# Kernel optimization log

Hardware: AMD Instinct MI355X
Metric: run time of the kernel (lower is better)

Reference implementation:

```python
import jax, jax.numpy as jnp
import numpy as np

B, S, N, M = 64, 512, 512, 128   # batch, sensory_size, state_size, motor_size
UNFOLDS = 6
DT = 0.1  # elapsed_time


def _gate(v, mu, sigma):
    # piecewise-linear 'sigmoid': clip((v - mu + sigma) / (2 sigma), 0, 1)
    # v: [B, P] -> [B, P, 1] broadcast against [P, N]
    return jnp.clip((v[..., None] - mu + sigma) / (2.0 * sigma), 0.0, 1.0)


def setup_inputs() -> dict:
    key = jax.random.key(0)
    ks = jax.random.split(key, 12)
    u = lambda k, sh, lo, hi: jax.random.uniform(k, sh, jnp.float32, lo, hi)
    inputs = jax.random.normal(ks[0], (B, S), dtype=jnp.float32)
    states = jax.random.normal(ks[1], (B, N), dtype=jnp.float32) * 0.1
    # parameters per _init_ranges
    tau = u(ks[2], (N,), 0.001, 2.0)
    b = u(ks[3], (N,), -0.2, 0.2)
    erev = jnp.where(jax.random.bernoulli(ks[4], 0.8, (N, N)), 1.0, -1.0).astype(jnp.float32)
    w = u(ks[5], (N, N), 0.001, 1.0)
    sigma = jnp.full((N, N), 0.5, jnp.float32)
    mu = jnp.full((N, N), 0.5, jnp.float32)
    sensory_erev = jnp.where(jax.random.bernoulli(ks[6], 0.8, (S, N)), 1.0, -1.0).astype(jnp.float32)
    sensory_w = u(ks[7], (S, N), 0.001, 1.0)
    sensory_sigma = jnp.full((S, N), 0.5, jnp.float32)
    sensory_mu = jnp.full((S, N), 0.5, jnp.float32)
    sparsity_mask = jax.random.bernoulli(ks[8], 0.3, (N, N)).astype(jnp.float32)
    sensory_sparsity_mask = jax.random.bernoulli(ks[9], 0.3, (S, N)).astype(jnp.float32)
    input_w = jnp.ones((S,), jnp.float32)
    input_b = jnp.zeros((S,), jnp.float32)
    output_w = jnp.ones((M,), jnp.float32)
    output_b = jnp.zeros((M,), jnp.float32)
    return dict(inputs=inputs, states=states, tau=tau, b=b, erev=erev, w=w,
                sigma=sigma, mu=mu, sensory_erev=sensory_erev, sensory_w=sensory_w,
                sensory_sigma=sensory_sigma, sensory_mu=sensory_mu,
                sparsity_mask=sparsity_mask, sensory_sparsity_mask=sensory_sparsity_mask,
                input_w=input_w, input_b=input_b, output_w=output_w, output_b=output_b)


def reference(inputs, states, tau, b, erev, w, sigma, mu,
              sensory_erev, sensory_w, sensory_sigma, sensory_mu,
              sparsity_mask, sensory_sparsity_mask,
              input_w, input_b, output_w, output_b):
    # input mapping (affine)
    x = inputs * input_w + input_b                                   # [B, S]
    # sensory synapses, computed once
    sa = _gate(x, sensory_mu, sensory_sigma) * sensory_sparsity_mask  # [B, S, N]
    s_rev = jnp.einsum('bsn,sn->bn', sa, sensory_erev)               # [B, N]
    s_w = jnp.einsum('bsn,sn->bn', sa, sensory_w)                    # [B, N]
    delta = DT / UNFOLDS

    def step(v, _):
        g = _gate(v, mu, sigma) * sparsity_mask                      # [B, N, N]
        sum_rev = jnp.einsum('bij,ij->bj', g, erev) + s_rev + b      # sum over presynaptic i
        sum_w = jnp.einsum('bij,ij->bj', g, w) + s_w
        k = 1.0 / (1.0 + sum_w)
        taun = tau * k
        q = taun / (taun + delta)
        v_new = q * v + (1.0 - q) * k * sum_rev
        return v_new, None

    v, _ = jax.lax.scan(step, states, None, length=UNFOLDS)
    # output mapping: slice last M neurons (M < N), then affine
    out = v[:, -M:] * output_w + output_b                            # [B, M]
    return out, v
```

## Files before the change

### kernel.cpp

```cpp
#include <hip/hip_runtime.h>
#include <string.h>

constexpr int cB = 64, cS = 512, cN = 512, cM = 128, cUNF = 6;
constexpr float cDELTA = 0.016666666666666666f;

constexpr int KB = 4;
constexpr int JT = 32;
constexpr int NJT = cN / JT;
constexpr int NT = 1024;
constexpr int NW = NT / 64;
constexpr int NB = (cB / KB) * NJT;
constexpr int ILEN = 16;
constexpr int SLEN = 16;

constexpr size_t OFF_EWT = 0;
constexpr size_t OFF_SRB = (size_t)cN * cN * 2;
constexpr size_t OFF_SW  = OFF_SRB + (size_t)cB * cN;
constexpr size_t OFF_VA  = OFF_SW  + (size_t)cB * cN;
constexpr size_t OFF_VB  = OFF_VA  + (size_t)cB * cN;
constexpr size_t OFF_CTR = OFF_VB  + (size_t)cB * cN;
constexpr int SLOT_STRIDE = 16;

__device__ __forceinline__ float clamp01(float x) {
    return __builtin_amdgcn_fmed3f(x, 0.0f, 1.0f);
}

__global__ __launch_bounds__(NT)
void k_prep(const float* __restrict__ inputs, const float* __restrict__ bias,
            const float* __restrict__ erev,  const float* __restrict__ wgt,
            const float* __restrict__ sigma, const float* __restrict__ mu,
            const float* __restrict__ serev, const float* __restrict__ swgt,
            const float* __restrict__ ssigma,const float* __restrict__ smu,
            const float* __restrict__ mask,  const float* __restrict__ smask,
            const float* __restrict__ inw,   const float* __restrict__ inb,
            float* __restrict__ ws)
{
    float2* EWt  = (float2*)(ws + OFF_EWT);
    float*  srb  = ws + OFF_SRB;
    float*  swS  = ws + OFF_SW;
    int*    ctr  = (int*)(ws + OFF_CTR);
    int*    flags = ctr + 4096;

    const int tid = threadIdx.x, bid = blockIdx.x;
    const int bg = bid >> 4, jt = bid & (NJT - 1);
    const int b0 = bg * KB, j0 = jt * JT;
    const int jl = tid & (JT - 1), ic = tid >> 5;
    const int wv_id = tid >> 6, lane = tid & 63;
    const int j = j0 + jl;

    __shared__ float xsh[cS * KB];
    __shared__ float redR[KB * NW * JT];
    __shared__ float redW[KB * NW * JT];

    {
        int idx = bid * NT + tid;
        int i = idx >> 9, jj = idx & (cN - 1);
        int jtt = jj >> 5, jjl = jj & (JT - 1);
        float mk = mask[idx];
        float2 ew = make_float2(erev[idx] * mk, wgt[idx] * mk);
        unsigned long long bits;
        memcpy(&bits, &ew, 8);
        __hip_atomic_store(
            (unsigned long long*)&EWt[(size_t)jtt * (cN * JT) + i * JT + jjl],
            bits, __ATOMIC_RELAXED, __HIP_MEMORY_SCOPE_AGENT);
        if (mk != 0.0f && !((sigma[idx] == 0.5f) && (mu[idx] == 0.5f)))
            __hip_atomic_store(&flags[jtt], 1, __ATOMIC_RELAXED, __HIP_MEMORY_SCOPE_AGENT);
    }

#pragma unroll
    for (int r = 0; r < (cS * KB) / NT; ++r) {
        int t = tid + r * NT;
        int bb = t & 3, s = t >> 2;
        xsh[t] = fmaf(inputs[(b0 + bb) * cS + s], inw[s], inb[s]);
    }
    __syncthreads();

    {
        float aR[KB] = {0.f, 0.f, 0.f, 0.f}, aW[KB] = {0.f, 0.f, 0.f, 0.f};
        int idx = (ic * SLEN) * cN + j;
        int xo  = (ic * SLEN) * KB;
#pragma unroll 4
        for (int ii = 0; ii < SLEN; ++ii, idx += cN, xo += KB) {
            float sg = ssigma[idx];
            float a  = 0.5f / sg;
            float c  = fmaf(-smu[idx], a, 0.5f);
            float mk = smask[idx];
            float e  = serev[idx] * mk;
            float wv = swgt[idx] * mk;
            const float4 xv = *(const float4*)&xsh[xo];
            float g;
            g = clamp01(fmaf(xv.x, a, c)); aR[0] = fmaf(g, e, aR[0]); aW[0] = fmaf(g, wv, aW[0]);
            g = clamp01(fmaf(xv.y, a, c)); aR[1] = fmaf(g, e, aR[1]); aW[1] = fmaf(g, wv, aW[1]);
            g = clamp01(fmaf(xv.z, a, c)); aR[2] = fmaf(g, e, aR[2]); aW[2] = fmaf(g, wv, aW[2]);
            g = clamp01(fmaf(xv.w, a, c)); aR[3] = fmaf(g, e, aR[3]); aW[3] = fmaf(g, wv, aW[3]);
        }
#pragma unroll
        for (int b = 0; b < KB; ++b) {
            aR[b] += __shfl_xor(aR[b], 32, 64);
            aW[b] += __shfl_xor(aW[b], 32, 64);
        }
        if (lane < JT) {
#pragma unroll
            for (int b = 0; b < KB; ++b) {
                redR[(b * NW + wv_id) * JT + lane] = aR[b];
                redW[(b * NW + wv_id) * JT + lane] = aW[b];
            }
        }
    }
    __syncthreads();

    if (tid < JT * KB) {
        int jj = tid & (JT - 1), bb = tid >> 5;
        float r = 0.f, wv = 0.f;
#pragma unroll
        for (int w = 0; w < NW; ++w) {
            r  += redR[(bb * NW + w) * JT + jj];
            wv += redW[(bb * NW + w) * JT + jj];
        }
        int jg = j0 + jj;
        int gidx = (b0 + bb) * cN + jg;
        srb[gidx] = r + bias[jg];
        swS[gidx] = wv;
    }
}

__global__ __launch_bounds__(NT, 4)
void k_main(const float* __restrict__ states, const float* __restrict__ tau,
            const float* __restrict__ sigma,  const float* __restrict__ mu,
            const float* __restrict__ outw,   const float* __restrict__ outb,
            float* __restrict__ out, float* __restrict__ ws)
{
    const float* srb = ws + OFF_SRB;
    const float* swS = ws + OFF_SW;
    float* vA  = ws + OFF_VA;
    float* vB  = ws + OFF_VB;
    int*   ctr = (int*)(ws + OFF_CTR);

    const int tid = threadIdx.x, bid = blockIdx.x;
    const int jt = (bid & 7) * 2 + ((bid >> 3) & 1);
    const int bg = bid >> 4;
    const int b0 = bg * KB, j0 = jt * JT;
    const int jl = tid & (JT - 1), ic = tid >> 5;
    const int wv_id = tid >> 6, lane = tid & 63;
    int* mySlot  = ctr + (bg * 16 + jt) * SLOT_STRIDE;
    int* bgSlots = ctr + (bg * 16) * SLOT_STRIDE;
    const int* flags = ctr + 4096;

    const float2* ews = (const float2*)(ws + OFF_EWT) + (size_t)jt * (cN * JT);

    __shared__ float stage[cN * KB];
    __shared__ float redR[KB * NW * JT];
    __shared__ float redW[KB * NW * JT];

    const int fast = (flags[jt] != 1);

    float my_srb = 0.f, my_sw = 0.f, my_tau = 0.f, my_ow = 0.f, my_ob = 0.f;
    float vold = 0.f;
    int my_gidx = 0, my_mi = -1;
    if (tid < JT * KB) {
        int jj = tid & (JT - 1), bb = tid >> 5;
        int jg = j0 + jj;
        my_gidx = (b0 + bb) * cN + jg;
        my_srb  = srb[my_gidx];
        my_sw   = swS[my_gidx];
        my_tau  = tau[jg];
        vold    = states[my_gidx];
        if (jg >= cN - cM) {
            int m = jg - (cN - cM);
            my_ow = outw[m]; my_ob = outb[m];
            my_mi = (b0 + bb) * cM + m;
        }
    }

    const float* vin = states;
    for (int u = 0; u < cUNF; ++u) {
#pragma unroll
        for (int r = 0; r < (cN * KB) / NT; ++r) {
            int t = tid + r * NT;
            int bb = t >> 9, ii = t & (cN - 1);
            float vvv = __hip_atomic_load(&vin[(b0 + bb) * cN + ii],
                                          __ATOMIC_RELAXED, __HIP_MEMORY_SCOPE_AGENT);
            stage[ii * KB + bb] = fast ? clamp01(vvv) : vvv;
        }
        __syncthreads();

        float aR[KB] = {0.f, 0.f, 0.f, 0.f}, aW[KB] = {0.f, 0.f, 0.f, 0.f};
        if (fast) {
            int eo = (ic * ILEN) * JT + jl;
            int vo = (ic * ILEN) * KB;
#pragma unroll 8
            for (int ii = 0; ii < ILEN; ++ii, eo += JT, vo += KB) {
                const float2 ew = ews[eo];
                const float4 g4 = *(const float4*)&stage[vo];
                aR[0] = fmaf(g4.x, ew.x, aR[0]); aW[0] = fmaf(g4.x, ew.y, aW[0]);
                aR[1] = fmaf(g4.y, ew.x, aR[1]); aW[1] = fmaf(g4.y, ew.y, aW[1]);
                aR[2] = fmaf(g4.z, ew.x, aR[2]); aW[2] = fmaf(g4.z, ew.y, aW[2]);
                aR[3] = fmaf(g4.w, ew.x, aR[3]); aW[3] = fmaf(g4.w, ew.y, aW[3]);
            }
        } else {
            int j    = j0 + jl;
            int idx  = (ic * ILEN) * cN + j;
            int eo   = (ic * ILEN) * JT + jl;
            int vo   = (ic * ILEN) * KB;
#pragma unroll 4
            for (int ii = 0; ii < ILEN; ++ii, idx += cN, eo += JT, vo += KB) {
                float sg = sigma[idx];
                float a  = 0.5f / sg;
                float c  = fmaf(-mu[idx], a, 0.5f);
                const float2 ew = ews[eo];
                const float4 v4 = *(const float4*)&stage[vo];
                float g;
                g = clamp01(fmaf(v4.x, a, c)); aR[0] = fmaf(g, ew.x, aR[0]); aW[0] = fmaf(g, ew.y, aW[0]);
                g = clamp01(fmaf(v4.y, a, c)); aR[1] = fmaf(g, ew.x, aR[1]); aW[1] = fmaf(g, ew.y, aW[1]);
                g = clamp01(fmaf(v4.z, a, c)); aR[2] = fmaf(g, ew.x, aR[2]); aW[2] = fmaf(g, ew.y, aW[2]);
                g = clamp01(fmaf(v4.w, a, c)); aR[3] = fmaf(g, ew.x, aR[3]); aW[3] = fmaf(g, ew.y, aW[3]);
            }
        }
#pragma unroll
        for (int b = 0; b < KB; ++b) {
            aR[b] += __shfl_xor(aR[b], 32, 64);
            aW[b] += __shfl_xor(aW[b], 32, 64);
        }
        if (lane < JT) {
#pragma unroll
            for (int b = 0; b < KB; ++b) {
                redR[(b * NW + wv_id) * JT + lane] = aR[b];
                redW[(b * NW + wv_id) * JT + lane] = aW[b];
            }
        }
        __syncthreads();

        float* vout = (u & 1) ? vB : vA;
        if (tid < JT * KB) {
            int jj = tid & (JT - 1), bb = tid >> 5;
            float r = 0.f, wv = 0.f;
#pragma unroll
            for (int w = 0; w < NW; ++w) {
                r  += redR[(bb * NW + w) * JT + jj];
                wv += redW[(bb * NW + w) * JT + jj];
            }
            r  += my_srb;
            wv += my_sw;
            float k    = 1.0f / (1.0f + wv);
            float taun = my_tau * k;
            float inv  = 1.0f / (taun + cDELTA);
            float vn   = (taun * inv) * vold + (cDELTA * inv) * k * r;
            vold = vn;
            if (u == cUNF - 1) {
                (out + cB * cM)[my_gidx] = vn;
                if (my_mi >= 0) out[my_mi] = fmaf(vn, my_ow, my_ob);
            } else {
                __hip_atomic_store(&vout[my_gidx], vn,
                                   __ATOMIC_RELAXED, __HIP_MEMORY_SCOPE_AGENT);
            }
        }

        if (u < cUNF - 1) {
            __syncthreads();
            if (tid == 0)
                __hip_atomic_store(mySlot, u + 1,
                                   __ATOMIC_RELAXED, __HIP_MEMORY_SCOPE_AGENT);
            if (tid < NJT) {
                const int* slot = bgSlots + tid * SLOT_STRIDE;
                while (__hip_atomic_load(slot, __ATOMIC_RELAXED, __HIP_MEMORY_SCOPE_AGENT) < u + 1)
                    __builtin_amdgcn_s_sleep(1);
            }
            __syncthreads();
            vin = (u & 1) ? vB : vA;
        }
    }
}

extern "C" void kernel_launch(void* const* d_in, const int* in_sizes, int n_in,
                              void* d_out, int out_size, void* d_ws, size_t ws_size,
                              hipStream_t stream)
{
    const float* inputs = (const float*)d_in[0];
    const float* states = (const float*)d_in[1];
    const float* tau    = (const float*)d_in[2];
    const float* bias   = (const float*)d_in[3];
    const float* erev   = (const float*)d_in[4];
    const float* wgt    = (const float*)d_in[5];
    const float* sigma  = (const float*)d_in[6];
    const float* mu     = (const float*)d_in[7];
    const float* serev  = (const float*)d_in[8];
    const float* swgt   = (const float*)d_in[9];
    const float* ssigma = (const float*)d_in[10];
    const float* smu    = (const float*)d_in[11];
    const float* mask   = (const float*)d_in[12];
    const float* smask  = (const float*)d_in[13];
    const float* inw    = (const float*)d_in[14];
    const float* inb    = (const float*)d_in[15];
    const float* outw   = (const float*)d_in[16];
    const float* outb   = (const float*)d_in[17];
    float* out = (float*)d_out;
    float* ws  = (float*)d_ws;

    k_prep<<<NB, NT, 0, stream>>>(inputs, bias, erev, wgt, sigma, mu,
                                  serev, swgt, ssigma, smu, mask, smask,
                                  inw, inb, ws);

    k_main<<<NB, NT, 0, stream>>>(states, tau, sigma, mu,
                                  outw, outb, out, ws);
}
```

Baseline: 124.1 us.

## Fuse prep and main into one MFMA fp16 kernel with register-resident weights

```diff
diff --git a/kernel.cpp b/kernel.cpp
--- a/kernel.cpp
+++ b/kernel.cpp
@@ -4,270 +4,248 @@
 constexpr int cB = 64, cS = 512, cN = 512, cM = 128, cUNF = 6;
 constexpr float cDELTA = 0.016666666666666666f;
 
-constexpr int KB = 4;
-constexpr int JT = 32;
-constexpr int NJT = cN / JT;
-constexpr int NT = 1024;
-constexpr int NW = NT / 64;
-constexpr int NB = (cB / KB) * NJT;
-constexpr int ILEN = 16;
-constexpr int SLEN = 16;
-
-constexpr size_t OFF_EWT = 0;
-constexpr size_t OFF_SRB = (size_t)cN * cN * 2;
-constexpr size_t OFF_SW  = OFF_SRB + (size_t)cB * cN;
-constexpr size_t OFF_VA  = OFF_SW  + (size_t)cB * cN;
-constexpr size_t OFF_VB  = OFF_VA  + (size_t)cB * cN;
-constexpr size_t OFF_CTR = OFF_VB  + (size_t)cB * cN;
+constexpr int JT   = 16;
+constexpr int NBLK = cN / JT;
+constexpr int NT   = 256;
 constexpr int SLOT_STRIDE = 16;
+
+constexpr size_t OFF_V0   = 0;
+constexpr size_t OFF_V1   = (size_t)cB * cN;
+constexpr size_t OFF_SLOT = OFF_V1 + (size_t)cB * cN;
+
+typedef _Float16 half8 __attribute__((ext_vector_type(8)));
+typedef float    floatx4 __attribute__((ext_vector_type(4)));
 
 __device__ __forceinline__ float clamp01(float x) {
     return __builtin_amdgcn_fmed3f(x, 0.0f, 1.0f);
 }
 
-__global__ __launch_bounds__(NT)
-void k_prep(const float* __restrict__ inputs, const float* __restrict__ bias,
-            const float* __restrict__ erev,  const float* __restrict__ wgt,
-            const float* __restrict__ sigma, const float* __restrict__ mu,
-            const float* __restrict__ serev, const float* __restrict__ swgt,
-            const float* __restrict__ ssigma,const float* __restrict__ smu,
-            const float* __restrict__ mask,  const float* __restrict__ smask,
-            const float* __restrict__ inw,   const float* __restrict__ inb,
-            float* __restrict__ ws)
+__global__ __launch_bounds__(NT, 1)
+void k_fused(const float* __restrict__ inputs, const float* __restrict__ states,
+             const float* __restrict__ tau,    const float* __restrict__ bias,
+             const float* __restrict__ erev,   const float* __restrict__ wgt,
+             const float* __restrict__ sigma,  const float* __restrict__ mu,
+             const float* __restrict__ serev,  const float* __restrict__ swgt,
+             const float* __restrict__ ssigma, const float* __restrict__ smu,
+             const float* __restrict__ mask,   const float* __restrict__ smask,
+             const float* __restrict__ inw,    const float* __restrict__ inb,
+             const float* __restrict__ outw,   const float* __restrict__ outb,
+             float* __restrict__ out, float* __restrict__ ws)
 {
-    float2* EWt  = (float2*)(ws + OFF_EWT);
-    float*  srb  = ws + OFF_SRB;
-    float*  swS  = ws + OFF_SW;
-    int*    ctr  = (int*)(ws + OFF_CTR);
-    int*    flags = ctr + 4096;
-
-    const int tid = threadIdx.x, bid = blockIdx.x;
-    const int bg = bid >> 4, jt = bid & (NJT - 1);
-    const int b0 = bg * KB, j0 = jt * JT;
-    const int jl = tid & (JT - 1), ic = tid >> 5;
-    const int wv_id = tid >> 6, lane = tid & 63;
-    const int j = j0 + jl;
-
-    __shared__ float xsh[cS * KB];
-    __shared__ float redR[KB * NW * JT];
-    __shared__ float redW[KB * NW * JT];
+    float* v0 = ws + OFF_V0;
+    float* v1 = ws + OFF_V1;
+    int* slots = (int*)(ws + OFF_SLOT);
+
+    const int tid  = threadIdx.x;
+    const int blk  = blockIdx.x;
+    const int j0   = blk * JT;
+    const int lane = tid & 63;
+    const int mt   = tid >> 6;
+    const int lr   = lane & 15;
+    const int lg   = lane >> 4;
+    const int bj   = j0 + lr;
+    const int arow = mt * 16 + lr;
+    const int kbase = lg * 8;
+    const int cb0  = mt * 16 + lg * 4;
+
+    int* mySlot = slots + blk * SLOT_STRIDE;
+    __shared__ int flagR, flagS;
+
+    float vold[4];
+    const float tau_j  = tau[bj];
+    const float bias_j = bias[bj];
+    float ow = 0.f, ob = 0.f;
+    if (bj >= cN - cM) { ow = outw[bj - (cN - cM)]; ob = outb[bj - (cN - cM)]; }
+
+#pragma unroll
+    for (int r = 0; r < 4; ++r) {
+        vold[r] = states[(size_t)(cb0 + r) * cN + bj];
+        __hip_atomic_store(&v0[(size_t)(cb0 + r) * cN + bj], vold[r],
+                           __ATOMIC_RELAXED, __HIP_MEMORY_SCOPE_AGENT);
+    }
+    if (tid == 0) { flagR = 0; flagS = 0; }
+    __syncthreads();
+    if (tid == 0)
+        __hip_atomic_store(mySlot, 1, __ATOMIC_RELAXED, __HIP_MEMORY_SCOPE_AGENT);
 
     {
-        int idx = bid * NT + tid;
-        int i = idx >> 9, jj = idx & (cN - 1);
-        int jtt = jj >> 5, jjl = jj & (JT - 1);
-        float mk = mask[idx];
-        float2 ew = make_float2(erev[idx] * mk, wgt[idx] * mk);
-        unsigned long long bits;
-        memcpy(&bits, &ew, 8);
-        __hip_atomic_store(
-            (unsigned long long*)&EWt[(size_t)jtt * (cN * JT) + i * JT + jjl],
-            bits, __ATOMIC_RELAXED, __HIP_MEMORY_SCOPE_AGENT);
-        if (mk != 0.0f && !((sigma[idx] == 0.5f) && (mu[idx] == 0.5f)))
-            __hip_atomic_store(&flags[jtt], 1, __ATOMIC_RELAXED, __HIP_MEMORY_SCOPE_AGENT);
-    }
-
-#pragma unroll
-    for (int r = 0; r < (cS * KB) / NT; ++r) {
-        int t = tid + r * NT;
-        int bb = t & 3, s = t >> 2;
-        xsh[t] = fmaf(inputs[(b0 + bb) * cS + s], inw[s], inb[s]);
+        bool badR = false, badS = false;
+        const int jj = j0 + (tid & 15);
+        const int i0 = (tid >> 4) * 32;
+        for (int r = 0; r < 32; ++r) {
+            size_t o = (size_t)(i0 + r) * cN + jj;
+            if (mask[o]  != 0.f && (sigma[o]  != 0.5f || mu[o]  != 0.5f)) badR = true;
+            if (smask[o] != 0.f && (ssigma[o] != 0.5f || smu[o] != 0.5f)) badS = true;
+        }
+        if (badR) flagR = 1;
+        if (badS) flagS = 1;
     }
     __syncthreads();
-
-    {
-        float aR[KB] = {0.f, 0.f, 0.f, 0.f}, aW[KB] = {0.f, 0.f, 0.f, 0.f};
-        int idx = (ic * SLEN) * cN + j;
-        int xo  = (ic * SLEN) * KB;
-#pragma unroll 4
-        for (int ii = 0; ii < SLEN; ++ii, idx += cN, xo += KB) {
-            float sg = ssigma[idx];
+    const bool fastR = (flagR == 0), fastS = (flagS == 0);
+
+    float srb[4], swv[4];
+    half8 bE[16], bW[16];
+    if (fastS) {
+#pragma unroll
+        for (int kk = 0; kk < 16; ++kk) {
+            half8 e8, w8;
+#pragma unroll
+            for (int t = 0; t < 8; ++t) {
+                size_t o = (size_t)(kk * 32 + kbase + t) * cN + bj;
+                float mk = smask[o];
+                e8[t] = (_Float16)(serev[o] * mk);
+                w8[t] = (_Float16)(swgt[o] * mk);
+            }
+            bE[kk] = e8; bW[kk] = w8;
+        }
+        floatx4 aR = {0.f, 0.f, 0.f, 0.f}, aW = {0.f, 0.f, 0.f, 0.f};
+#pragma unroll
+        for (int kk = 0; kk < 16; ++kk) {
+            const float* xp = inputs + (size_t)arow * cS + kk * 32 + kbase;
+            const float* wp = inw + kk * 32 + kbase;
+            const float* bp = inb + kk * 32 + kbase;
+            half8 ax;
+#pragma unroll
+            for (int t = 0; t < 8; ++t)
+                ax[t] = (_Float16)clamp01(fmaf(xp[t], wp[t], bp[t]));
+            aR = __builtin_amdgcn_mfma_f32_16x16x32_f16(ax, bE[kk], aR, 0, 0, 0);
+            aW = __builtin_amdgcn_mfma_f32_16x16x32_f16(ax, bW[kk], aW, 0, 0, 0);
+        }
+#pragma unroll
+        for (int r = 0; r < 4; ++r) { srb[r] = aR[r] + bias_j; swv[r] = aW[r]; }
+    } else {
+        float sr4[4] = {0,0,0,0}, sw4[4] = {0,0,0,0};
+        for (int s = 0; s < cS; ++s) {
+            size_t o = (size_t)s * cN + bj;
+            float mk = smask[o];
+            float sg = ssigma[o];
             float a  = 0.5f / sg;
-            float c  = fmaf(-smu[idx], a, 0.5f);
-            float mk = smask[idx];
-            float e  = serev[idx] * mk;
-            float wv = swgt[idx] * mk;
-            const float4 xv = *(const float4*)&xsh[xo];
-            float g;
-            g = clamp01(fmaf(xv.x, a, c)); aR[0] = fmaf(g, e, aR[0]); aW[0] = fmaf(g, wv, aW[0]);
-            g = clamp01(fmaf(xv.y, a, c)); aR[1] = fmaf(g, e, aR[1]); aW[1] = fmaf(g, wv, aW[1]);
-            g = clamp01(fmaf(xv.z, a, c)); aR[2] = fmaf(g, e, aR[2]); aW[2] = fmaf(g, wv, aW[2]);
-            g = clamp01(fmaf(xv.w, a, c)); aR[3] = fmaf(g, e, aR[3]); aW[3] = fmaf(g, wv, aW[3]);
-        }
-#pragma unroll
-        for (int b = 0; b < KB; ++b) {
-            aR[b] += __shfl_xor(aR[b], 32, 64);
-            aW[b] += __shfl_xor(aW[b], 32, 64);
-        }
-        if (lane < JT) {
-#pragma unroll
-            for (int b = 0; b < KB; ++b) {
-                redR[(b * NW + wv_id) * JT + lane] = aR[b];
-                redW[(b * NW + wv_id) * JT + lane] = aW[b];
-            }
-        }
+            float c  = fmaf(-smu[o], a, 0.5f);
+            float ee = serev[o] * mk, ww = swgt[o] * mk;
+            float iw = inw[s], ib = inb[s];
+#pragma unroll
+            for (int r = 0; r < 4; ++r) {
+                float x = fmaf(inputs[(size_t)(cb0 + r) * cS + s], iw, ib);
+                float g = clamp01(fmaf(x, a, c));
+                sr4[r] = fmaf(g, ee, sr4[r]);
+                sw4[r] = fmaf(g, ww, sw4[r]);
+            }
+        }
+#pragma unroll
+        for (int r = 0; r < 4; ++r) { srb[r] = sr4[r] + bias_j; swv[r] = sw4[r]; }
+    }
+
+    if (fastR) {
+#pragma unroll
+        for (int kk = 0; kk < 16; ++kk) {
+            half8 e8, w8;
+#pragma unroll
+            for (int t = 0; t < 8; ++t) {
+                size_t o = (size_t)(kk * 32 + kbase + t) * cN + bj;
+                float mk = mask[o];
+                e8[t] = (_Float16)(erev[o] * mk);
+                w8[t] = (_Float16)(wgt[o] * mk);
+            }
+            bE[kk] = e8; bW[kk] = w8;
+        }
+    }
+
+    if (tid < NBLK) {
+        const int* sl = slots + tid * SLOT_STRIDE;
+        while (__hip_atomic_load(sl, __ATOMIC_RELAXED, __HIP_MEMORY_SCOPE_AGENT) < 1)
+            __builtin_amdgcn_s_sleep(1);
     }
     __syncthreads();
 
-    if (tid < JT * KB) {
-        int jj = tid & (JT - 1), bb = tid >> 5;
-        float r = 0.f, wv = 0.f;
-#pragma unroll
-        for (int w = 0; w < NW; ++w) {
-            r  += redR[(bb * NW + w) * JT + jj];
-            wv += redW[(bb * NW + w) * JT + jj];
-        }
-        int jg = j0 + jj;
-        int gidx = (b0 + bb) * cN + jg;
-        srb[gidx] = r + bias[jg];
-        swS[gidx] = wv;
-    }
-}
-
-__global__ __launch_bounds__(NT, 4)
-void k_main(const float* __restrict__ states, const float* __restrict__ tau,
-            const float* __restrict__ sigma,  const float* __restrict__ mu,
-            const float* __restrict__ outw,   const float* __restrict__ outb,
-            float* __restrict__ out, float* __restrict__ ws)
-{
-    const float* srb = ws + OFF_SRB;
-    const float* swS = ws + OFF_SW;
-    float* vA  = ws + OFF_VA;
-    float* vB  = ws + OFF_VB;
-    int*   ctr = (int*)(ws + OFF_CTR);
-
-    const int tid = threadIdx.x, bid = blockIdx.x;
-    const int jt = (bid & 7) * 2 + ((bid >> 3) & 1);
-    const int bg = bid >> 4;
-    const int b0 = bg * KB, j0 = jt * JT;
-    const int jl = tid & (JT - 1), ic = tid >> 5;
-    const int wv_id = tid >> 6, lane = tid & 63;
-    int* mySlot  = ctr + (bg * 16 + jt) * SLOT_STRIDE;
-    int* bgSlots = ctr + (bg * 16) * SLOT_STRIDE;
-    const int* flags = ctr + 4096;
-
-    const float2* ews = (const float2*)(ws + OFF_EWT) + (size_t)jt * (cN * JT);
-
-    __shared__ float stage[cN * KB];
-    __shared__ float redR[KB * NW * JT];
-    __shared__ float redW[KB * NW * JT];
-
-    const int fast = (flags[jt] != 1);
-
-    float my_srb = 0.f, my_sw = 0.f, my_tau = 0.f, my_ow = 0.f, my_ob = 0.f;
-    float vold = 0.f;
-    int my_gidx = 0, my_mi = -1;
-    if (tid < JT * KB) {
-        int jj = tid & (JT - 1), bb = tid >> 5;
-        int jg = j0 + jj;
-        my_gidx = (b0 + bb) * cN + jg;
-        my_srb  = srb[my_gidx];
-        my_sw   = swS[my_gidx];
-        my_tau  = tau[jg];
-        vold    = states[my_gidx];
-        if (jg >= cN - cM) {
-            int m = jg - (cN - cM);
-            my_ow = outw[m]; my_ob = outb[m];
-            my_mi = (b0 + bb) * cM + m;
-        }
-    }
-
-    const float* vin = states;
     for (int u = 0; u < cUNF; ++u) {
-#pragma unroll
-        for (int r = 0; r < (cN * KB) / NT; ++r) {
-            int t = tid + r * NT;
-            int bb = t >> 9, ii = t & (cN - 1);
-            float vvv = __hip_atomic_load(&vin[(b0 + bb) * cN + ii],
-                                          __ATOMIC_RELAXED, __HIP_MEMORY_SCOPE_AGENT);
-            stage[ii * KB + bb] = fast ? clamp01(vvv) : vvv;
-        }
-        __syncthreads();
-
-        float aR[KB] = {0.f, 0.f, 0.f, 0.f}, aW[KB] = {0.f, 0.f, 0.f, 0.f};
-        if (fast) {
-            int eo = (ic * ILEN) * JT + jl;
-            int vo = (ic * ILEN) * KB;
-#pragma unroll 8
-            for (int ii = 0; ii < ILEN; ++ii, eo += JT, vo += KB) {
-                const float2 ew = ews[eo];
-                const float4 g4 = *(const float4*)&stage[vo];
-                aR[0] = fmaf(g4.x, ew.x, aR[0]); aW[0] = fmaf(g4.x, ew.y, aW[0]);
-                aR[1] = fmaf(g4.y, ew.x, aR[1]); aW[1] = fmaf(g4.y, ew.y, aW[1]);
-                aR[2] = fmaf(g4.z, ew.x, aR[2]); aW[2] = fmaf(g4.z, ew.y, aW[2]);
-                aR[3] = fmaf(g4.w, ew.x, aR[3]); aW[3] = fmaf(g4.w, ew.y, aW[3]);
-            }
+        const float* vR = (u & 1) ? v1 : v0;
+        float*       vW = (u & 1) ? v0 : v1;
+
+        float sumE[4], sumW[4];
+        if (fastR) {
+            half8 ax[16];
+#pragma unroll
+            for (int kk = 0; kk < 16; ++kk) {
+                union { unsigned long long u[4]; float f[8]; } cv;
+                const unsigned long long* p = (const unsigned long long*)
+                    (vR + (size_t)arow * cN + kk * 32 + kbase);
+                cv.u[0] = __hip_atomic_load(p + 0, __ATOMIC_RELAXED, __HIP_MEMORY_SCOPE_AGENT);
+                cv.u[1] = __hip_atomic_load(p + 1, __ATOMIC_RELAXED, __HIP_MEMORY_SCOPE_AGENT);
+                cv.u[2] = __hip_atomic_load(p + 2, __ATOMIC_RELAXED, __HIP_MEMORY_SCOPE_AGENT);
+                cv.u[3] = __hip_atomic_load(p + 3, __ATOMIC_RELAXED, __HIP_MEMORY_SCOPE_AGENT);
+                half8 a8;
+#pragma unroll
+                for (int t = 0; t < 8; ++t)
+                    a8[t] = (_Float16)clamp01(cv.f[t]);
+                ax[kk] = a8;
+            }
+            floatx4 aE = {0.f, 0.f, 0.f, 0.f}, aWc = {0.f, 0.f, 0.f, 0.f};
+#pragma unroll
+            for (int kk = 0; kk < 16; ++kk) {
+                aE  = __builtin_amdgcn_mfma_f32_16x16x32_f16(ax[kk], bE[kk], aE,  0, 0, 0);
+                aWc = __builtin_amdgcn_mfma_f32_16x16x32_f16(ax[kk], bW[kk], aWc, 0, 0, 0);
+            }
+#pragma unroll
+            for (int r = 0; r < 4; ++r) { sumE[r] = aE[r]; sumW[r] = aWc[r]; }
         } else {
-            int j    = j0 + jl;
-            int idx  = (ic * ILEN) * cN + j;
-            int eo   = (ic * ILEN) * JT + jl;
-            int vo   = (ic * ILEN) * KB;
-#pragma unroll 4
-            for (int ii = 0; ii < ILEN; ++ii, idx += cN, eo += JT, vo += KB) {
-                float sg = sigma[idx];
+            float r4[4] = {0,0,0,0}, w4[4] = {0,0,0,0};
+            for (int i = 0; i < cN; ++i) {
+                size_t o = (size_t)i * cN + bj;
+                float mk = mask[o];
+                float sg = sigma[o];
                 float a  = 0.5f / sg;
-                float c  = fmaf(-mu[idx], a, 0.5f);
-                const float2 ew = ews[eo];
-                const float4 v4 = *(const float4*)&stage[vo];
-                float g;
-                g = clamp01(fmaf(v4.x, a, c)); aR[0] = fmaf(g, ew.x, aR[0]); aW[0] = fmaf(g, ew.y, aW[0]);
-                g = clamp01(fmaf(v4.y, a, c)); aR[1] = fmaf(g, ew.x, aR[1]); aW[1] = fmaf(g, ew.y, aW[1]);
-                g = clamp01(fmaf(v4.z, a, c)); aR[2] = fmaf(g, ew.x, aR[2]); aW[2] = fmaf(g, ew.y, aW[2]);
-                g = clamp01(fmaf(v4.w, a, c)); aR[3] = fmaf(g, ew.x, aR[3]); aW[3] = fmaf(g, ew.y, aW[3]);
-            }
-        }
-#pragma unroll
-        for (int b = 0; b < KB; ++b) {
-            aR[b] += __shfl_xor(aR[b], 32, 64);
-            aW[b] += __shfl_xor(aW[b], 32, 64);
-        }
-        if (lane < JT) {
-#pragma unroll
-            for (int b = 0; b < KB; ++b) {
-                redR[(b * NW + wv_id) * JT + lane] = aR[b];
-                redW[(b * NW + wv_id) * JT + lane] = aW[b];
-            }
-        }
-        __syncthreads();
-
-        float* vout = (u & 1) ? vB : vA;
-        if (tid < JT * KB) {
-            int jj = tid & (JT - 1), bb = tid >> 5;
-            float r = 0.f, wv = 0.f;
-#pragma unroll
-            for (int w = 0; w < NW; ++w) {
-                r  += redR[(bb * NW + w) * JT + jj];
-                wv += redW[(bb * NW + w) * JT + jj];
-            }
-            r  += my_srb;
-            wv += my_sw;
-            float k    = 1.0f / (1.0f + wv);
-            float taun = my_tau * k;
+                float c  = fmaf(-mu[o], a, 0.5f);
+                float ee = erev[o] * mk, ww = wgt[o] * mk;
+#pragma unroll
+                for (int r = 0; r < 4; ++r) {
+                    float vi = __hip_atomic_load(&vR[(size_t)(cb0 + r) * cN + i],
+                                                 __ATOMIC_RELAXED, __HIP_MEMORY_SCOPE_AGENT);
+                    float g = clamp01(fmaf(vi, a, c));
+                    r4[r] = fmaf(g, ee, r4[r]);
+                    w4[r] = fmaf(g, ww, w4[r]);
+                }
+            }
+#pragma unroll
+            for (int r = 0; r < 4; ++r) { sumE[r] = r4[r]; sumW[r] = w4[r]; }
+        }
+
+#pragma unroll
+        for (int r = 0; r < 4; ++r) {
+            float rr   = sumE[r] + srb[r];
+            float wsum = sumW[r] + swv[r];
+            float k    = 1.0f / (1.0f + wsum);
+            float taun = tau_j * k;
             float inv  = 1.0f / (taun + cDELTA);
-            float vn   = (taun * inv) * vold + (cDELTA * inv) * k * r;
-            vold = vn;
-            if (u == cUNF - 1) {
-                (out + cB * cM)[my_gidx] = vn;
-                if (my_mi >= 0) out[my_mi] = fmaf(vn, my_ow, my_ob);
-            } else {
-                __hip_atomic_store(&vout[my_gidx], vn,
+            float vn   = (taun * inv) * vold[r] + (cDELTA * inv) * k * rr;
+            vold[r] = vn;
+        }
+
+        if (u < cUNF - 1) {
+#pragma unroll
+            for (int r = 0; r < 4; ++r)
+                __hip_atomic_store(&vW[(size_t)(cb0 + r) * cN + bj], vold[r],
                                    __ATOMIC_RELAXED, __HIP_MEMORY_SCOPE_AGENT);
-            }
-        }
-
-        if (u < cUNF - 1) {
             __syncthreads();
             if (tid == 0)
-                __hip_atomic_store(mySlot, u + 1,
+                __hip_atomic_store(mySlot, u + 2,
                                    __ATOMIC_RELAXED, __HIP_MEMORY_SCOPE_AGENT);
-            if (tid < NJT) {
-                const int* slot = bgSlots + tid * SLOT_STRIDE;
-                while (__hip_atomic_load(slot, __ATOMIC_RELAXED, __HIP_MEMORY_SCOPE_AGENT) < u + 1)
+            if (tid < NBLK) {
+                const int* sl = slots + tid * SLOT_STRIDE;
+                while (__hip_atomic_load(sl, __ATOMIC_RELAXED,
+                                         __HIP_MEMORY_SCOPE_AGENT) < u + 2)
                     __builtin_amdgcn_s_sleep(1);
             }
             __syncthreads();
-            vin = (u & 1) ? vB : vA;
-        }
+        }
+    }
+
+    float* vout = out + (size_t)cB * cM;
+#pragma unroll
+    for (int r = 0; r < 4; ++r) {
+        int b = cb0 + r;
+        vout[(size_t)b * cN + bj] = vold[r];
+        if (bj >= cN - cM)
+            out[(size_t)b * cM + (bj - (cN - cM))] = fmaf(vold[r], ow, ob);
     }
 }
 
@@ -296,10 +274,8 @@
     float* out = (float*)d_out;
     float* ws  = (float*)d_ws;
 
-    k_prep<<<NB, NT, 0, stream>>>(inputs, bias, erev, wgt, sigma, mu,
-                                  serev, swgt, ssigma, smu, mask, smask,
-                                  inw, inb, ws);
-
-    k_main<<<NB, NT, 0, stream>>>(states, tau, sigma, mu,
-                                  outw, outb, out, ws);
+    k_fused<<<NBLK, NT, 0, stream>>>(inputs, states, tau, bias, erev, wgt,
+                                     sigma, mu, serev, swgt, ssigma, smu,
+                                     mask, smask, inw, inb, outw, outb,
+                                     out, ws);
 }
```

Result: slower. 240.6 us (+93.9%).
